# Kernel optimization log

Measured on AMD Instinct MI355X. Metric: run time of the kernel, lower is better.

Reference implementation:

```python
import jax, jax.numpy as jnp
import numpy as np

B = 4
S = 2_000_000
NPIX = 196608  # 12 * 128**2 (HEALPix nside=128)


def setup_inputs() -> dict:
    key = jax.random.key(0)
    k1, k2, k3, k4 = jax.random.split(key, 4)
    tod = jax.random.normal(k1, (B, S), dtype=jnp.float32)
    # per-sample Stokes weights (I, Q, U) of the pointing matrix rows
    weights = jax.random.normal(k2, (S, 3), dtype=jnp.float32)
    projection_cov = jax.random.uniform(k3, (NPIX,), dtype=jnp.float32)
    pix_idx = jax.random.randint(k4, (S,), 0, NPIX, dtype=jnp.int32)
    return {"tod": tod, "weights": weights, "projection_cov": projection_cov,
            "pix_idx": pix_idx}


def reference(tod, weights, projection_cov, pix_idx):
    npix = projection_cov.shape[0]
    # P^T: scatter-add each TOD sample's Stokes contribution into its pixel.
    # contrib: [B, S, 3]
    contrib = tod[:, :, None] * weights[None, :, :]
    sky = jax.vmap(
        lambda c: jax.ops.segment_sum(c, pix_idx, num_segments=npix)
    )(contrib)  # [B, npix, 3]
    # coverage normalization of I, Q, U
    sky = sky / projection_cov[None, :, None]
    return sky
```

## Files before the change

kernel.cpp:

```cpp
#include <hip/hip_runtime.h>


constexpr int NB   = 256;
constexpr int BW   = 768;
constexpr int NBLK = 1024;
constexpr int TILE = 2048;


__device__ __forceinline__ unsigned f2bf(float f) {
    unsigned u = __float_as_uint(f);
    unsigned r = ((u >> 16) & 1u) + 0x7fffu;
    return (u + r) >> 16;
}
__device__ __forceinline__ float bf_lo(unsigned u) {
    return __uint_as_float(u << 16);
}
__device__ __forceinline__ float bf_hi(unsigned u) {
    return __uint_as_float(u & 0xffff0000u);
}


__global__ __launch_bounds__(512)
void hist_kernel(const int* __restrict__ pix, int S, int chunk,
                 int* __restrict__ hist2d) {
    __shared__ int lh[NB];
    for (int t = threadIdx.x; t < NB; t += blockDim.x) lh[t] = 0;
    __syncthreads();
    const int beg = blockIdx.x * chunk;
    const int end = min(S, beg + chunk);
    for (int j = beg + threadIdx.x; j < end; j += blockDim.x)
        atomicAdd(&lh[pix[j] / BW], 1);
    __syncthreads();
    for (int t = threadIdx.x; t < NB; t += blockDim.x)
        hist2d[(size_t)blockIdx.x * NB + t] = lh[t];
}

__global__ __launch_bounds__(NBLK)
void scan_blocks_kernel(int* __restrict__ hist2d,
                        int* __restrict__ btotal) {
    __shared__ int sc[NBLK];
    const int bkt = blockIdx.x, tid = threadIdx.x;
    const int v = hist2d[(size_t)tid * NB + bkt];
    sc[tid] = v;
    __syncthreads();
    for (int off = 1; off < NBLK; off <<= 1) {
        int x = (tid >= off) ? sc[tid - off] : 0;
        __syncthreads();
        sc[tid] += x;
        __syncthreads();
    }
    hist2d[(size_t)tid * NB + bkt] = sc[tid] - v;
    if (tid == NBLK - 1) btotal[bkt] = sc[tid];
}

__global__ __launch_bounds__(NB)
void scan_buckets_kernel(const int* __restrict__ btotal,
                         int* __restrict__ bbase, int S) {
    __shared__ int sc[NB];
    const int tid = threadIdx.x;
    const int v = btotal[tid];
    sc[tid] = v;
    __syncthreads();
    for (int off = 1; off < NB; off <<= 1) {
        int x = (tid >= off) ? sc[tid - off] : 0;
        __syncthreads();
        sc[tid] += x;
        __syncthreads();
    }
    bbase[tid] = sc[tid] - v;
    if (tid == NB - 1) bbase[NB] = sc[tid];
}

__global__ __launch_bounds__(512)
void reorder_sorted_kernel(const float* __restrict__ tod,
                           const float* __restrict__ weights,
                           const int* __restrict__ pix,
                           int S, int chunk,
                           const int* __restrict__ hist2d,
                           const int* __restrict__ bbase,
                           uint4* __restrict__ rec) {
    __shared__ uint4          lrec[TILE];
    __shared__ unsigned short lbk[TILE];
    __shared__ unsigned short lidx[TILE];
    __shared__ int            lcur[NB];
    __shared__ int            lstart[NB];
    __shared__ int            lbase[NB];

    const int blk = blockIdx.x;
    const int beg = blk * chunk;
    const int end = min(S, beg + chunk);
    const int n = end - beg;

    if (threadIdx.x < NB) {
        lcur[threadIdx.x] = 0;
        lbase[threadIdx.x] = bbase[threadIdx.x]
                           + hist2d[(size_t)blk * NB + threadIdx.x];
    }
    __syncthreads();

    for (int jj = threadIdx.x; jj < n; jj += blockDim.x) {
        const int j = beg + jj;
        const int p = pix[j];
        const int bkt = p / BW;
        const int lp  = p - bkt * BW;
        const float w0 = weights[3 * j + 0];
        const float w1 = weights[3 * j + 1];
        const float w2 = weights[3 * j + 2];
        const float t0 = tod[(size_t)0 * S + j];
        const float t1 = tod[(size_t)1 * S + j];
        const float t2 = tod[(size_t)2 * S + j];
        const float t3 = tod[(size_t)3 * S + j];
        uint4 v;
        v.x = f2bf(w0) | (f2bf(w1) << 16);
        v.y = f2bf(w2) | ((unsigned)lp << 16);
        v.z = f2bf(t0) | (f2bf(t1) << 16);
        v.w = f2bf(t2) | (f2bf(t3) << 16);
        lrec[jj] = v;
        lbk[jj] = (unsigned short)bkt;
        atomicAdd(&lcur[bkt], 1);
    }
    __syncthreads();

    if (threadIdx.x < 64) {
        const int i0 = threadIdx.x * 4;
        const int a0 = lcur[i0], a1 = lcur[i0 + 1];
        const int a2 = lcur[i0 + 2], a3 = lcur[i0 + 3];
        const int t1 = a0 + a1, t2 = t1 + a2, t3 = t2 + a3;
        int x = t3;
        #pragma unroll
        for (int off = 1; off < 64; off <<= 1) {
            const int y = __shfl_up(x, off, 64);
            if ((int)threadIdx.x >= off) x += y;
        }
        const int base = x - t3;
        lstart[i0]     = base;
        lstart[i0 + 1] = base + a0;
        lstart[i0 + 2] = base + t1;
        lstart[i0 + 3] = base + t2;
        lcur[i0]     = base;
        lcur[i0 + 1] = base + a0;
        lcur[i0 + 2] = base + t1;
        lcur[i0 + 3] = base + t2;
    }
    __syncthreads();

    for (int jj = threadIdx.x; jj < n; jj += blockDim.x) {
        const int r = atomicAdd(&lcur[lbk[jj]], 1);
        lidx[r] = (unsigned short)jj;
    }
    __syncthreads();

    for (int r = threadIdx.x; r < n; r += blockDim.x) {
        const int jj = lidx[r];
        const int bkt = lbk[jj];
        const int dst = lbase[bkt] + (r - lstart[bkt]);
        rec[dst] = lrec[jj];
    }
}

__global__ __launch_bounds__(1024)
void accum_sort_kernel(const uint4* __restrict__ rec,
                       const float* __restrict__ cov,
                       const int* __restrict__ bbase,
                       float* __restrict__ out,
                       int npix) {
    __shared__ uint4          lrec[TILE];
    __shared__ unsigned short lpx[TILE];
    __shared__ unsigned short lidx[TILE];
    __shared__ int            start[BW + 1];
    __shared__ int            cur[BW];

    const int bkt = blockIdx.x;
    const int beg = bbase[bkt], end = bbase[bkt + 1];
    const int l = threadIdx.x & 255;
    const int q = threadIdx.x >> 8;
    float s00 = 0.f, s01 = 0.f, s02 = 0.f;
    float s10 = 0.f, s11 = 0.f, s12 = 0.f;
    float s20 = 0.f, s21 = 0.f, s22 = 0.f;

    for (int tbeg = beg; tbeg < end; tbeg += TILE) {
        const int n = min(TILE, end - tbeg);

        for (int t = threadIdx.x; t < BW; t += blockDim.x) cur[t] = 0;
        __syncthreads();
        for (int j = threadIdx.x; j < n; j += blockDim.x) {
            const uint4 r = rec[(size_t)(tbeg + j)];
            lrec[j] = r;
            const int lp = (int)(r.y >> 16);
            lpx[j] = (unsigned short)lp;
            atomicAdd(&cur[lp], 1);
        }
        __syncthreads();

        if (threadIdx.x < 64) {
            const int i0 = threadIdx.x * 12;
            int v[12], pre[12], run = 0;
            #pragma unroll
            for (int k = 0; k < 12; ++k) {
                v[k] = cur[i0 + k]; pre[k] = run; run += v[k];
            }
            int x = run;
            #pragma unroll
            for (int off = 1; off < 64; off <<= 1) {
                const int y = __shfl_up(x, off, 64);
                if ((int)threadIdx.x >= off) x += y;
            }
            const int base = x - run;
            #pragma unroll
            for (int k = 0; k < 12; ++k) {
                start[i0 + k] = base + pre[k];
                cur[i0 + k]   = base + pre[k];
            }
            if (threadIdx.x == 63) start[BW] = base + run;
        }
        __syncthreads();

        for (int j = threadIdx.x; j < n; j += blockDim.x) {
            const int r = atomicAdd(&cur[lpx[j]], 1);
            lidx[r] = (unsigned short)j;
        }
        __syncthreads();

        {
            const int rb = start[l], re = start[l + 1];
            for (int j = rb; j < re; ++j) {
                const int i = lidx[j];
                const uint4 r = lrec[i];
                const float tq = (q == 0) ? bf_lo(r.z) : (q == 1) ? bf_hi(r.z)
                               : (q == 2) ? bf_lo(r.w) : bf_hi(r.w);
                s00 += tq * bf_lo(r.x);
                s01 += tq * bf_hi(r.x);
                s02 += tq * bf_lo(r.y);
            }
        }
        {
            const int rb = start[l + 256], re = start[l + 257];
            for (int j = rb; j < re; ++j) {
                const int i = lidx[j];
                const uint4 r = lrec[i];
                const float tq = (q == 0) ? bf_lo(r.z) : (q == 1) ? bf_hi(r.z)
                               : (q == 2) ? bf_lo(r.w) : bf_hi(r.w);
                s10 += tq * bf_lo(r.x);
                s11 += tq * bf_hi(r.x);
                s12 += tq * bf_lo(r.y);
            }
        }
        {
            const int rb = start[l + 512], re = start[l + 513];
            for (int j = rb; j < re; ++j) {
                const int i = lidx[j];
                const uint4 r = lrec[i];
                const float tq = (q == 0) ? bf_lo(r.z) : (q == 1) ? bf_hi(r.z)
                               : (q == 2) ? bf_lo(r.w) : bf_hi(r.w);
                s20 += tq * bf_lo(r.x);
                s21 += tq * bf_hi(r.x);
                s22 += tq * bf_lo(r.y);
            }
        }
        __syncthreads();
    }

    {
        const int p = bkt * BW + l;
        const float rc = 1.0f / cov[p];
        const size_t o = ((size_t)q * npix + p) * 3;
        out[o + 0] = s00 * rc; out[o + 1] = s01 * rc; out[o + 2] = s02 * rc;
    }
    {
        const int p = bkt * BW + 256 + l;
        const float rc = 1.0f / cov[p];
        const size_t o = ((size_t)q * npix + p) * 3;
        out[o + 0] = s10 * rc; out[o + 1] = s11 * rc; out[o + 2] = s12 * rc;
    }
    {
        const int p = bkt * BW + 512 + l;
        const float rc = 1.0f / cov[p];
        const size_t o = ((size_t)q * npix + p) * 3;
        out[o + 0] = s20 * rc; out[o + 1] = s21 * rc; out[o + 2] = s22 * rc;
    }
}


__global__ void zero_out_kernel(float4* __restrict__ out, int n4) {
    int i = blockIdx.x * blockDim.x + threadIdx.x;
    int stride = gridDim.x * blockDim.x;
    for (; i < n4; i += stride) out[i] = make_float4(0.f, 0.f, 0.f, 0.f);
}

__global__ void scatter_kernel(const float* __restrict__ tod,
                               const float* __restrict__ weights,
                               const int*   __restrict__ pix,
                               float* __restrict__ out,
                               int S, int npix, int B) {
    int i = blockIdx.x * blockDim.x + threadIdx.x;
    int stride = gridDim.x * blockDim.x;
    const size_t bstride = (size_t)npix * 3;
    for (int s = i; s < S; s += stride) {
        const int p = pix[s];
        const float w0 = weights[3 * s + 0];
        const float w1 = weights[3 * s + 1];
        const float w2 = weights[3 * s + 2];
        float* o = out + (size_t)p * 3;
        for (int b = 0; b < B; ++b) {
            const float t = tod[(size_t)b * S + s];
            float* ob = o + (size_t)b * bstride;
            atomicAdd(ob + 0, t * w0);
            atomicAdd(ob + 1, t * w1);
            atomicAdd(ob + 2, t * w2);
        }
    }
}

__global__ void normalize_kernel(float* __restrict__ out,
                                 const float* __restrict__ cov,
                                 int npix, int B) {
    int i = blockIdx.x * blockDim.x + threadIdx.x;
    int stride = gridDim.x * blockDim.x;
    const int total = B * npix;
    for (; i < total; i += stride) {
        const int p = i % npix;
        const float c = cov[p];
        float* o = out + (size_t)i * 3;
        o[0] /= c; o[1] /= c; o[2] /= c;
    }
}


extern "C" void kernel_launch(void* const* d_in, const int* in_sizes, int n_in,
                              void* d_out, int out_size, void* d_ws, size_t ws_size,
                              hipStream_t stream) {
    const float* tod     = (const float*)d_in[0];
    const float* weights = (const float*)d_in[1];
    const float* cov     = (const float*)d_in[2];
    const int*   pix     = (const int*)d_in[3];
    float* out = (float*)d_out;

    const int S    = in_sizes[3];
    const int npix = in_sizes[2];
    const int B    = in_sizes[0] / S;

    const size_t meta_ints  = (size_t)NB * NBLK + NB + (NB + 1);
    const size_t meta_bytes = ((meta_ints * sizeof(int)) + 63) & ~(size_t)63;
    const size_t need_rec   = meta_bytes + (size_t)S * 16;

    const int chunk = (S + NBLK - 1) / NBLK;

    if (B == 4 && npix == NB * BW && chunk <= TILE && ws_size >= need_rec) {
        int* hist2d = (int*)d_ws;
        int* btotal = hist2d + (size_t)NB * NBLK;
        int* bbase  = btotal + NB;
        uint4* rec  = (uint4*)((char*)d_ws + meta_bytes);

        hist_kernel<<<NBLK, 512, 0, stream>>>(pix, S, chunk, hist2d);
        scan_blocks_kernel<<<NB, NBLK, 0, stream>>>(hist2d, btotal);
        scan_buckets_kernel<<<1, NB, 0, stream>>>(btotal, bbase, S);
        reorder_sorted_kernel<<<NBLK, 512, 0, stream>>>(tod, weights, pix, S,
                                                        chunk, hist2d, bbase, rec);
        accum_sort_kernel<<<NB, 1024, 0, stream>>>(rec, cov, bbase, out, npix);
        return;
    }

    const int block = 256;
    {
        const int n4 = out_size / 4;
        int grid = min((n4 + block - 1) / block, 2048);
        zero_out_kernel<<<grid, block, 0, stream>>>((float4*)out, n4);
    }
    {
        int grid = min((S + block - 1) / block, 4096);
        scatter_kernel<<<grid, block, 0, stream>>>(tod, weights, pix, out, S, npix, B);
    }
    {
        const int total = B * npix;
        int grid = min((total + block - 1) / block, 2048);
        normalize_kernel<<<grid, block, 0, stream>>>(out, cov, npix, B);
    }
}
```

Before: 73.78 us.

## Replace shared-memory local sort in reorder with direct atomic-slot scatter

The reorder kernel no longer stages a tile in LDS, scans local bucket counts and writes records in sorted order. Each thread now claims a slot with an LDS atomic and writes its packed record straight to global memory, with the next sample's loads software-prefetched. Block count drops from 1024 to 256 with 1024 threads each, so each block covers a larger chunk and the TILE size limit is removed. The global writes become scattered rather than coalesced per bucket, and record order within a bucket is now nondeterministic, which can change the floating-point summation order.

```diff
diff --git a/kernel.cpp b/kernel.cpp
--- a/kernel.cpp
+++ b/kernel.cpp
@@ -3,7 +3,7 @@
 
 constexpr int NB   = 256;
 constexpr int BW   = 768;
-constexpr int NBLK = 1024;
+constexpr int NBLK = 256;
 constexpr int TILE = 2048;
 
 
@@ -20,19 +20,19 @@
 }
 
 
-__global__ __launch_bounds__(512)
+__global__ __launch_bounds__(1024)
 void hist_kernel(const int* __restrict__ pix, int S, int chunk,
                  int* __restrict__ hist2d) {
     __shared__ int lh[NB];
-    for (int t = threadIdx.x; t < NB; t += blockDim.x) lh[t] = 0;
+    if (threadIdx.x < NB) lh[threadIdx.x] = 0;
     __syncthreads();
     const int beg = blockIdx.x * chunk;
     const int end = min(S, beg + chunk);
     for (int j = beg + threadIdx.x; j < end; j += blockDim.x)
         atomicAdd(&lh[pix[j] / BW], 1);
     __syncthreads();
-    for (int t = threadIdx.x; t < NB; t += blockDim.x)
-        hist2d[(size_t)blockIdx.x * NB + t] = lh[t];
+    if (threadIdx.x < NB)
+        hist2d[(size_t)blockIdx.x * NB + threadIdx.x] = lh[threadIdx.x];
 }
 
 __global__ __launch_bounds__(NBLK)
@@ -71,90 +71,59 @@
     if (tid == NB - 1) bbase[NB] = sc[tid];
 }
 
-__global__ __launch_bounds__(512)
-void reorder_sorted_kernel(const float* __restrict__ tod,
+__global__ __launch_bounds__(1024)
+void reorder_linear_kernel(const float* __restrict__ tod,
                            const float* __restrict__ weights,
                            const int* __restrict__ pix,
                            int S, int chunk,
                            const int* __restrict__ hist2d,
                            const int* __restrict__ bbase,
                            uint4* __restrict__ rec) {
-    __shared__ uint4          lrec[TILE];
-    __shared__ unsigned short lbk[TILE];
-    __shared__ unsigned short lidx[TILE];
-    __shared__ int            lcur[NB];
-    __shared__ int            lstart[NB];
-    __shared__ int            lbase[NB];
-
+    __shared__ int lbase[NB];
+    __shared__ int lcur[NB];
     const int blk = blockIdx.x;
+    if (threadIdx.x < NB) {
+        lbase[threadIdx.x] = bbase[threadIdx.x]
+                           + hist2d[(size_t)blk * NB + threadIdx.x];
+        lcur[threadIdx.x] = 0;
+    }
+    __syncthreads();
     const int beg = blk * chunk;
     const int end = min(S, beg + chunk);
-    const int n = end - beg;
-
-    if (threadIdx.x < NB) {
-        lcur[threadIdx.x] = 0;
-        lbase[threadIdx.x] = bbase[threadIdx.x]
-                           + hist2d[(size_t)blk * NB + threadIdx.x];
-    }
-    __syncthreads();
-
-    for (int jj = threadIdx.x; jj < n; jj += blockDim.x) {
-        const int j = beg + jj;
-        const int p = pix[j];
+    const int bs  = blockDim.x;
+
+    int j = beg + (int)threadIdx.x;
+    int p = 0;
+    float w0 = 0, w1 = 0, w2 = 0, t0 = 0, t1 = 0, t2 = 0, t3 = 0;
+    if (j < end) {
+        p  = pix[j];
+        w0 = weights[3 * j + 0]; w1 = weights[3 * j + 1]; w2 = weights[3 * j + 2];
+        t0 = tod[(size_t)0 * S + j]; t1 = tod[(size_t)1 * S + j];
+        t2 = tod[(size_t)2 * S + j]; t3 = tod[(size_t)3 * S + j];
+    }
+    while (j < end) {
+        const int jn = j + bs;
+        int pn = 0;
+        float wn0 = 0, wn1 = 0, wn2 = 0, tn0 = 0, tn1 = 0, tn2 = 0, tn3 = 0;
+        if (jn < end) {
+            pn  = pix[jn];
+            wn0 = weights[3 * jn + 0]; wn1 = weights[3 * jn + 1]; wn2 = weights[3 * jn + 2];
+            tn0 = tod[(size_t)0 * S + jn]; tn1 = tod[(size_t)1 * S + jn];
+            tn2 = tod[(size_t)2 * S + jn]; tn3 = tod[(size_t)3 * S + jn];
+        }
         const int bkt = p / BW;
         const int lp  = p - bkt * BW;
-        const float w0 = weights[3 * j + 0];
-        const float w1 = weights[3 * j + 1];
-        const float w2 = weights[3 * j + 2];
-        const float t0 = tod[(size_t)0 * S + j];
-        const float t1 = tod[(size_t)1 * S + j];
-        const float t2 = tod[(size_t)2 * S + j];
-        const float t3 = tod[(size_t)3 * S + j];
+        const int r   = atomicAdd(&lcur[bkt], 1);
+        const int dst = lbase[bkt] + r;
         uint4 v;
         v.x = f2bf(w0) | (f2bf(w1) << 16);
         v.y = f2bf(w2) | ((unsigned)lp << 16);
         v.z = f2bf(t0) | (f2bf(t1) << 16);
         v.w = f2bf(t2) | (f2bf(t3) << 16);
-        lrec[jj] = v;
-        lbk[jj] = (unsigned short)bkt;
-        atomicAdd(&lcur[bkt], 1);
-    }
-    __syncthreads();
-
-    if (threadIdx.x < 64) {
-        const int i0 = threadIdx.x * 4;
-        const int a0 = lcur[i0], a1 = lcur[i0 + 1];
-        const int a2 = lcur[i0 + 2], a3 = lcur[i0 + 3];
-        const int t1 = a0 + a1, t2 = t1 + a2, t3 = t2 + a3;
-        int x = t3;
-        #pragma unroll
-        for (int off = 1; off < 64; off <<= 1) {
-            const int y = __shfl_up(x, off, 64);
-            if ((int)threadIdx.x >= off) x += y;
-        }
-        const int base = x - t3;
-        lstart[i0]     = base;
-        lstart[i0 + 1] = base + a0;
-        lstart[i0 + 2] = base + t1;
-        lstart[i0 + 3] = base + t2;
-        lcur[i0]     = base;
-        lcur[i0 + 1] = base + a0;
-        lcur[i0 + 2] = base + t1;
-        lcur[i0 + 3] = base + t2;
-    }
-    __syncthreads();
-
-    for (int jj = threadIdx.x; jj < n; jj += blockDim.x) {
-        const int r = atomicAdd(&lcur[lbk[jj]], 1);
-        lidx[r] = (unsigned short)jj;
-    }
-    __syncthreads();
-
-    for (int r = threadIdx.x; r < n; r += blockDim.x) {
-        const int jj = lidx[r];
-        const int bkt = lbk[jj];
-        const int dst = lbase[bkt] + (r - lstart[bkt]);
-        rec[dst] = lrec[jj];
+        rec[dst] = v;
+        j = jn; p = pn;
+        w0 = wn0; w1 = wn1; w2 = wn2;
+        t0 = tn0; t1 = tn1; t2 = tn2; t3 = tn3;
     }
 }
 
@@ -345,17 +314,17 @@
 
     const int chunk = (S + NBLK - 1) / NBLK;
 
-    if (B == 4 && npix == NB * BW && chunk <= TILE && ws_size >= need_rec) {
+    if (B == 4 && npix == NB * BW && ws_size >= need_rec) {
         int* hist2d = (int*)d_ws;
         int* btotal = hist2d + (size_t)NB * NBLK;
         int* bbase  = btotal + NB;
         uint4* rec  = (uint4*)((char*)d_ws + meta_bytes);
 
-        hist_kernel<<<NBLK, 512, 0, stream>>>(pix, S, chunk, hist2d);
+        hist_kernel<<<NBLK, 1024, 0, stream>>>(pix, S, chunk, hist2d);
         scan_blocks_kernel<<<NB, NBLK, 0, stream>>>(hist2d, btotal);
         scan_buckets_kernel<<<1, NB, 0, stream>>>(btotal, bbase, S);
-        reorder_sorted_kernel<<<NBLK, 512, 0, stream>>>(tod, weights, pix, S,
-                                                        chunk, hist2d, bbase, rec);
+        reorder_linear_kernel<<<NBLK, 1024, 0, stream>>>(tod, weights, pix, S,
+                                                         chunk, hist2d, bbase, rec);
         accum_sort_kernel<<<NB, 1024, 0, stream>>>(rec, cov, bbase, out, npix);
         return;
     }
```

After: 69.87 us. -5.3%, faster.

## Use fewer, larger sort blocks that loop over sub-tiles during reorder

Applied to the files above, without the earlier changes.

Cuts the number of partition blocks from 1024 to 256 and raises their thread count to 1024. Each reorder block now walks its larger chunk in tiles of 3072 samples and advances its per-bucket output bases after each tile. Staging records are held in shared memory as four separate word arrays instead of uint4. The goal is to shrink the hist2d matrix and the cost of the block-scan, and to lower per-block overhead. The trade-off is fewer blocks for 256 CUs, more barriers per block, and shorter contiguous runs per bucket in each scatter.

```diff
diff --git a/kernel.cpp b/kernel.cpp
--- a/kernel.cpp
+++ b/kernel.cpp
@@ -3,8 +3,9 @@
 
 constexpr int NB   = 256;
 constexpr int BW   = 768;
-constexpr int NBLK = 1024;
+constexpr int NBLK = 256;
 constexpr int TILE = 2048;
+constexpr int RT   = 3072;
 
 
 __device__ __forceinline__ unsigned f2bf(float f) {
@@ -20,19 +21,19 @@
 }
 
 
-__global__ __launch_bounds__(512)
+__global__ __launch_bounds__(1024)
 void hist_kernel(const int* __restrict__ pix, int S, int chunk,
                  int* __restrict__ hist2d) {
     __shared__ int lh[NB];
-    for (int t = threadIdx.x; t < NB; t += blockDim.x) lh[t] = 0;
+    if (threadIdx.x < NB) lh[threadIdx.x] = 0;
     __syncthreads();
     const int beg = blockIdx.x * chunk;
     const int end = min(S, beg + chunk);
     for (int j = beg + threadIdx.x; j < end; j += blockDim.x)
         atomicAdd(&lh[pix[j] / BW], 1);
     __syncthreads();
-    for (int t = threadIdx.x; t < NB; t += blockDim.x)
-        hist2d[(size_t)blockIdx.x * NB + t] = lh[t];
+    if (threadIdx.x < NB)
+        hist2d[(size_t)blockIdx.x * NB + threadIdx.x] = lh[threadIdx.x];
 }
 
 __global__ __launch_bounds__(NBLK)
@@ -71,7 +72,7 @@
     if (tid == NB - 1) bbase[NB] = sc[tid];
 }
 
-__global__ __launch_bounds__(512)
+__global__ __launch_bounds__(1024)
 void reorder_sorted_kernel(const float* __restrict__ tod,
                            const float* __restrict__ weights,
                            const int* __restrict__ pix,
@@ -79,82 +80,90 @@
                            const int* __restrict__ hist2d,
                            const int* __restrict__ bbase,
                            uint4* __restrict__ rec) {
-    __shared__ uint4          lrec[TILE];
-    __shared__ unsigned short lbk[TILE];
-    __shared__ unsigned short lidx[TILE];
+    __shared__ unsigned       lrx[RT], lry[RT], lrz[RT], lrw[RT];
+    __shared__ unsigned short lbk[RT];
+    __shared__ unsigned short lidx[RT];
+    __shared__ int            lbase[NB];
     __shared__ int            lcur[NB];
     __shared__ int            lstart[NB];
-    __shared__ int            lbase[NB];
 
     const int blk = blockIdx.x;
-    const int beg = blk * chunk;
-    const int end = min(S, beg + chunk);
-    const int n = end - beg;
-
     if (threadIdx.x < NB) {
-        lcur[threadIdx.x] = 0;
         lbase[threadIdx.x] = bbase[threadIdx.x]
                            + hist2d[(size_t)blk * NB + threadIdx.x];
     }
-    __syncthreads();
-
-    for (int jj = threadIdx.x; jj < n; jj += blockDim.x) {
-        const int j = beg + jj;
-        const int p = pix[j];
-        const int bkt = p / BW;
-        const int lp  = p - bkt * BW;
-        const float w0 = weights[3 * j + 0];
-        const float w1 = weights[3 * j + 1];
-        const float w2 = weights[3 * j + 2];
-        const float t0 = tod[(size_t)0 * S + j];
-        const float t1 = tod[(size_t)1 * S + j];
-        const float t2 = tod[(size_t)2 * S + j];
-        const float t3 = tod[(size_t)3 * S + j];
-        uint4 v;
-        v.x = f2bf(w0) | (f2bf(w1) << 16);
-        v.y = f2bf(w2) | ((unsigned)lp << 16);
-        v.z = f2bf(t0) | (f2bf(t1) << 16);
-        v.w = f2bf(t2) | (f2bf(t3) << 16);
-        lrec[jj] = v;
-        lbk[jj] = (unsigned short)bkt;
-        atomicAdd(&lcur[bkt], 1);
-    }
-    __syncthreads();
-
-    if (threadIdx.x < 64) {
-        const int i0 = threadIdx.x * 4;
-        const int a0 = lcur[i0], a1 = lcur[i0 + 1];
-        const int a2 = lcur[i0 + 2], a3 = lcur[i0 + 3];
-        const int t1 = a0 + a1, t2 = t1 + a2, t3 = t2 + a3;
-        int x = t3;
-        #pragma unroll
-        for (int off = 1; off < 64; off <<= 1) {
-            const int y = __shfl_up(x, off, 64);
-            if ((int)threadIdx.x >= off) x += y;
-        }
-        const int base = x - t3;
-        lstart[i0]     = base;
-        lstart[i0 + 1] = base + a0;
-        lstart[i0 + 2] = base + t1;
-        lstart[i0 + 3] = base + t2;
-        lcur[i0]     = base;
-        lcur[i0 + 1] = base + a0;
-        lcur[i0 + 2] = base + t1;
-        lcur[i0 + 3] = base + t2;
-    }
-    __syncthreads();
-
-    for (int jj = threadIdx.x; jj < n; jj += blockDim.x) {
-        const int r = atomicAdd(&lcur[lbk[jj]], 1);
-        lidx[r] = (unsigned short)jj;
-    }
-    __syncthreads();
-
-    for (int r = threadIdx.x; r < n; r += blockDim.x) {
-        const int jj = lidx[r];
-        const int bkt = lbk[jj];
-        const int dst = lbase[bkt] + (r - lstart[bkt]);
-        rec[dst] = lrec[jj];
+    const int cbeg = blk * chunk;
+    const int cend = min(S, cbeg + chunk);
+    __syncthreads();
+
+    for (int tbeg = cbeg; tbeg < cend; tbeg += RT) {
+        const int n = min(RT, cend - tbeg);
+
+        if (threadIdx.x < NB) lcur[threadIdx.x] = 0;
+        __syncthreads();
+
+        for (int jj = threadIdx.x; jj < n; jj += blockDim.x) {
+            const int j = tbeg + jj;
+            const int p = pix[j];
+            const int bkt = p / BW;
+            const int lp  = p - bkt * BW;
+            const float w0 = weights[3 * j + 0];
+            const float w1 = weights[3 * j + 1];
+            const float w2 = weights[3 * j + 2];
+            const float t0 = tod[(size_t)0 * S + j];
+            const float t1 = tod[(size_t)1 * S + j];
+            const float t2 = tod[(size_t)2 * S + j];
+            const float t3 = tod[(size_t)3 * S + j];
+            lrx[jj] = f2bf(w0) | (f2bf(w1) << 16);
+            lry[jj] = f2bf(w2) | ((unsigned)lp << 16);
+            lrz[jj] = f2bf(t0) | (f2bf(t1) << 16);
+            lrw[jj] = f2bf(t2) | (f2bf(t3) << 16);
+            lbk[jj] = (unsigned short)bkt;
+            atomicAdd(&lcur[bkt], 1);
+        }
+        __syncthreads();
+
+        if (threadIdx.x < 64) {
+            const int i0 = threadIdx.x * 4;
+            const int a0 = lcur[i0], a1 = lcur[i0 + 1];
+            const int a2 = lcur[i0 + 2], a3 = lcur[i0 + 3];
+            const int t1 = a0 + a1, t2 = t1 + a2, t3 = t2 + a3;
+            int x = t3;
+            #pragma unroll
+            for (int off = 1; off < 64; off <<= 1) {
+                const int y = __shfl_up(x, off, 64);
+                if ((int)threadIdx.x >= off) x += y;
+            }
+            const int base = x - t3;
+            lstart[i0]     = base;
+            lstart[i0 + 1] = base + a0;
+            lstart[i0 + 2] = base + t1;
+            lstart[i0 + 3] = base + t2;
+            lcur[i0]     = base;
+            lcur[i0 + 1] = base + a0;
+            lcur[i0 + 2] = base + t1;
+            lcur[i0 + 3] = base + t2;
+        }
+        __syncthreads();
+
+        for (int jj = threadIdx.x; jj < n; jj += blockDim.x) {
+            const int r = atomicAdd(&lcur[lbk[jj]], 1);
+            lidx[r] = (unsigned short)jj;
+        }
+        __syncthreads();
+
+        for (int r = threadIdx.x; r < n; r += blockDim.x) {
+            const int jj  = lidx[r];
+            const int bkt = lbk[jj];
+            uint4 v;
+            v.x = lrx[jj]; v.y = lry[jj]; v.z = lrz[jj]; v.w = lrw[jj];
+            rec[(size_t)(lbase[bkt] + (r - lstart[bkt]))] = v;
+        }
+        __syncthreads();
+
+        if (threadIdx.x < NB)
+            lbase[threadIdx.x] += lcur[threadIdx.x] - lstart[threadIdx.x];
+        __syncthreads();
     }
 }
 
@@ -345,17 +354,17 @@
 
     const int chunk = (S + NBLK - 1) / NBLK;
 
-    if (B == 4 && npix == NB * BW && chunk <= TILE && ws_size >= need_rec) {
+    if (B == 4 && npix == NB * BW && ws_size >= need_rec) {
         int* hist2d = (int*)d_ws;
         int* btotal = hist2d + (size_t)NB * NBLK;
         int* bbase  = btotal + NB;
         uint4* rec  = (uint4*)((char*)d_ws + meta_bytes);
 
-        hist_kernel<<<NBLK, 512, 0, stream>>>(pix, S, chunk, hist2d);
+        hist_kernel<<<NBLK, 1024, 0, stream>>>(pix, S, chunk, hist2d);
         scan_blocks_kernel<<<NB, NBLK, 0, stream>>>(hist2d, btotal);
         scan_buckets_kernel<<<1, NB, 0, stream>>>(btotal, bbase, S);
-        reorder_sorted_kernel<<<NBLK, 512, 0, stream>>>(tod, weights, pix, S,
-                                                        chunk, hist2d, bbase, rec);
+        reorder_sorted_kernel<<<NBLK, 1024, 0, stream>>>(tod, weights, pix, S,
+                                                         chunk, hist2d, bbase, rec);
         accum_sort_kernel<<<NB, 1024, 0, stream>>>(rec, cov, bbase, out, npix);
         return;
     }
```

New measurement: 71.08 us. -3.7%, faster.
